# Performance work log

Measured on AMD Instinct MI355X. Metric: run time of the kernel, lower is better.

Reference implementation:

```python
import jax, jax.numpy as jnp
import numpy as np

B, T, A, H, E = 512, 64, 32, 512, 32


def sinusoidal_pos_encoding(t, dim):
    # t: (B, T) float positions -> (B, T, dim)
    half = dim // 2
    freqs = jnp.exp(-jnp.log(10000.0) * jnp.arange(half, dtype=jnp.float32) / half)
    ang = t[..., None] * freqs  # (B, T, half)
    return jnp.concatenate([jnp.sin(ang), jnp.cos(ang)], axis=-1)


def cat_linear(x, W, b, cat_ids):
    # x: (B, T, Din); W: (E, Din, Dout); b: (E, Dout); cat_ids: (B,)
    Wg = W[cat_ids]            # (B, Din, Dout) gathered per-sample weights
    bg = b[cat_ids][:, None]   # (B, 1, Dout)
    return jnp.einsum('btd,bdh->bth', x, Wg) + bg


def swish(x):
    return x * jax.nn.sigmoid(x)


def setup_inputs() -> dict:
    key = jax.random.key(0)
    ks = jax.random.split(key, 10)
    s = lambda fan_in: 1.0 / np.sqrt(fan_in)
    return {
        'actions': jax.random.normal(ks[0], (B, T, A), dtype=jnp.float32),
        'timesteps': jax.random.uniform(ks[1], (B,), dtype=jnp.float32),
        'cat_ids': jax.random.randint(ks[2], (B,), 0, E),
        'W1': jax.random.normal(ks[3], (E, A, H), dtype=jnp.float32) * s(A),
        'b1': jnp.zeros((E, H), dtype=jnp.float32),
        'W2': jax.random.normal(ks[4], (E, 2 * H, H), dtype=jnp.float32) * s(2 * H),
        'b2': jnp.zeros((E, H), dtype=jnp.float32),
        'W3': jax.random.normal(ks[5], (E, H, H), dtype=jnp.float32) * s(H),
        'b3': jnp.zeros((E, H), dtype=jnp.float32),
    }


def reference(actions, timesteps, cat_ids, W1, b1, W2, b2, W3, b3):
    b, t, _ = actions.shape
    timesteps_bt = jnp.broadcast_to(timesteps[:, None], (b, t))
    a_emb = cat_linear(actions, W1, b1, cat_ids)              # (B, T, H)
    tau_emb = sinusoidal_pos_encoding(timesteps_bt, H).astype(a_emb.dtype)
    x = jnp.concatenate([a_emb, tau_emb], axis=-1)            # (B, T, 2H)
    x = swish(cat_linear(x, W2, b2, cat_ids))                 # (B, T, H)
    x = cat_linear(x, W3, b3, cat_ids)                        # (B, T, H)
    return x
```

## Files before the change

kernel.cpp:

```cpp
#include <hip/hip_runtime.h>
#include <hip/hip_bf16.h>

#define B_ 512
#define T_ 64
#define A_ 32
#define H_ 512
#define E_ 32
#define MAX_TASKS 272
#define CAP_ 168
#define GRID_ (8 * CAP_)
#define SC 16

typedef unsigned short u16;
typedef unsigned int u32;
typedef __attribute__((ext_vector_type(8))) short short8;
typedef __attribute__((ext_vector_type(4))) float floatx4;

static __device__ __forceinline__ u16 f2bf(float f) {
    u32 u = __builtin_bit_cast(u32, f);
    u += 0x7fffu + ((u >> 16) & 1u);
    return (u16)(u >> 16);
}

static __device__ __forceinline__ void gl2lds16(const u16* g, u16* l) {
    __builtin_amdgcn_global_load_lds(
        (const __attribute__((address_space(1))) void*)g,
        (__attribute__((address_space(3))) void*)l, 16, 0, 0);
}

__global__ void group_kernel(const int* __restrict__ cat_ids,
                             int* __restrict__ sample_list,
                             int4* __restrict__ tasks,
                             int* __restrict__ itemlist,
                             int* __restrict__ eoff_g,
                             int* __restrict__ ecnt_g) {
    __shared__ int cnt[E_], off[E_], cur[E_], toff[E_], jc[8];
    __shared__ int total, fb;
    int tid = threadIdx.x;
    if (tid < E_) { cnt[tid] = 0; cur[tid] = 0; }
    __syncthreads();
    int e = cat_ids[tid];
    atomicAdd(&cnt[e], 1);
    __syncthreads();
    if (tid == 0) {
        int run = 0, trun = 0;
        for (int i = 0; i < E_; i++) {
            off[i] = run;  run += cnt[i];
            toff[i] = trun; trun += (cnt[i] + 1) >> 1;
        }
        total = trun;
    }
    __syncthreads();
    if (tid < E_) {
        int c = cnt[tid], o = off[tid], to = toff[tid];
        eoff_g[tid] = o;
        ecnt_g[tid] = c;
        for (int j = 0; j < c; j += 2)
            tasks[to++] = make_int4(tid, o + j, (c - j >= 2) ? 2 : 1, 0);
    }
    if (tid < 8) {
        int J = 0;
        for (int cc = 0; cc < 4; cc++) J += 4 * ((cnt[tid + 8 * cc] + 1) >> 1);
        jc[tid] = J;
    }
    __syncthreads();
    if (tid == 0) {
        int f = 0;
        for (int x = 0; x < 8; x++) if (jc[x] > CAP_) f = 1;
        fb = f;
    }
    __syncthreads();
    if (!fb) {
        if (tid < 8) {
            int j = 0;
            for (int cc = 0; cc < 4; cc++) {
                int ee = tid + 8 * cc;
                int nt = (cnt[ee] + 1) >> 1, t0 = toff[ee];
                for (int t = t0; t < t0 + nt; t++)
                    for (int nb = 0; nb < 4; nb++) {
                        itemlist[tid + 8 * j] = (t << 2) | nb;
                        j++;
                    }
            }
            for (; j < CAP_; j++) itemlist[tid + 8 * j] = -1;
        }
    } else {
        for (int f = tid; f < GRID_; f += 512)
            itemlist[f] = (f < 4 * total) ? f : -1;
    }
    int p = atomicAdd(&cur[e], 1);
    sample_list[off[e] + p] = tid;
}

__global__ __launch_bounds__(256) void embed_kernel(
        const float* __restrict__ actions, const int* __restrict__ cat_ids,
        const float* __restrict__ W1, const float* __restrict__ b1,
        u16* __restrict__ a_emb) {
    int b = blockIdx.x;
    int tid = threadIdx.x;
    int e = cat_ids[b];

    __shared__ float act[T_ * A_];
    const float* asrc = actions + (size_t)b * T_ * A_;
    for (int i = tid; i < T_ * A_; i += 256) act[i] = asrc[i];
    __syncthreads();

    const float* w1 = W1 + (size_t)e * A_ * H_;
    int n0 = tid, n1 = tid + 256;
    float wA[A_], wB[A_];
#pragma unroll
    for (int k = 0; k < A_; k++) {
        wA[k] = w1[k * H_ + n0];
        wB[k] = w1[k * H_ + n1];
    }
    float bA = b1[e * H_ + n0], bB = b1[e * H_ + n1];
    u16* orow = a_emb + (size_t)b * T_ * H_;
    for (int tt = 0; tt < T_; tt++) {
        float accA = bA, accB = bB;
#pragma unroll
        for (int k = 0; k < A_; k++) {
            float a = act[tt * A_ + k];
            accA = fmaf(a, wA[k], accA);
            accB = fmaf(a, wB[k], accB);
        }
        orow[tt * H_ + n0] = f2bf(accA);
        orow[tt * H_ + n1] = f2bf(accB);
    }
}

__global__ __launch_bounds__(256) void convert_transpose(
        const float* __restrict__ W, u16* __restrict__ Wt, int srcK, int dstK) {
    int n = blockIdx.y * 256 + threadIdx.x;
    int k0 = blockIdx.x * 32;
    int e = blockIdx.z;
    const float* src = W + ((size_t)e * srcK + k0) * H_ + n;
    short8 out[4];
#pragma unroll
    for (int j = 0; j < 32; j++)
        out[j >> 3][j & 7] = (short)f2bf(src[(size_t)j * H_]);
    u16* dst = Wt + ((size_t)e * H_ + n) * dstK + k0;
#pragma unroll
    for (int c = 0; c < 4; c++) *(short8*)(dst + c * 8) = out[c];
}

__global__ __launch_bounds__(256) void tau_bias_kernel(
        const float* __restrict__ W2, const float* __restrict__ b2,
        const float* __restrict__ timesteps, const int* __restrict__ sample_list,
        const int* __restrict__ eoff, const int* __restrict__ ecnt,
        float* __restrict__ bias2s) {
    int cc = blockIdx.x;
    int e = blockIdx.y;
    int cnt = ecnt[e], off = eoff[e];
    if (cnt == 0) return;
    int tid = threadIdx.x;
    int kq = tid >> 6, lane = tid & 63;
    int n = cc * 64 + lane;
    __shared__ float tauS[SC][512];
    __shared__ float pS[4][SC][64];
    const float* wb = W2 + ((size_t)e * 1024 + 512) * H_;

    for (int c0 = 0; c0 < cnt; c0 += SC) {
        for (int i = tid; i < SC * 512; i += 256) {
            int sl = i >> 9, k = i & 511;
            float v = 0.f;
            if (c0 + sl < cnt) {
                int s = sample_list[off + c0 + sl];
                float tval = timesteps[s];
                int kk = k & 255;
                float freq = expf(-9.210340371976184f * (float)kk * (1.0f / 256.0f));
                float ang = tval * freq;
                v = (k < 256) ? sinf(ang) : cosf(ang);
            }
            tauS[sl][k] = v;
        }
        __syncthreads();

        float a[SC];
#pragma unroll
        for (int s = 0; s < SC; s++) a[s] = 0.f;
        int kb = kq * 128;
        for (int k = kb; k < kb + 128; k += 4) {
            float w0 = wb[(size_t)k * H_ + n];
            float w1 = wb[(size_t)(k + 1) * H_ + n];
            float w2 = wb[(size_t)(k + 2) * H_ + n];
            float w3 = wb[(size_t)(k + 3) * H_ + n];
#pragma unroll
            for (int s = 0; s < SC; s++) {
                float4 t4 = *(const float4*)&tauS[s][k];
                a[s] = fmaf(t4.x, w0, a[s]);
                a[s] = fmaf(t4.y, w1, a[s]);
                a[s] = fmaf(t4.z, w2, a[s]);
                a[s] = fmaf(t4.w, w3, a[s]);
            }
        }
#pragma unroll
        for (int s = 0; s < SC; s++) pS[kq][s][lane] = a[s];
        __syncthreads();

        for (int o = tid; o < SC * 64; o += 256) {
            int sl = o >> 6, ln = o & 63;
            if (c0 + sl < cnt) {
                float v = pS[0][sl][ln] + pS[1][sl][ln] +
                          pS[2][sl][ln] + pS[3][sl][ln];
                int s = sample_list[off + c0 + sl];
                int col = cc * 64 + ln;
                bias2s[(size_t)s * H_ + col] = v + b2[e * H_ + col];
            }
        }
        __syncthreads();
    }
}

template <int DIN, bool PSBIAS, bool DO_SWISH, bool OUT_BF16>
__global__ __launch_bounds__(256, 2) void moe_gemm(
        const u16* __restrict__ xsrc, const u16* __restrict__ Wt,
        const float* __restrict__ bias,
        const int* __restrict__ sample_list, const int4* __restrict__ tasks,
        const int* __restrict__ itemlist, void* __restrict__ outp) {
    int item = itemlist[blockIdx.x];
    if (item < 0) return;
    int4 task = tasks[item >> 2];
    int nb = item & 3;
    int ns = task.z;
    int e = task.x;
    int s0 = sample_list[task.y];
    int s1 = (ns > 1) ? sample_list[task.y + 1] : s0;
    int n0 = nb * 128;

    int tid = threadIdx.x;
    int lane = tid & 63, wv = tid >> 6;
    int wr = wv >> 1, wc = wv & 1;
    int quad = lane >> 4, c15 = lane & 15;
    int r8 = lane >> 3, cg = lane & 7;

    __shared__ __align__(16) u16 xs[2][128 * 64];
    __shared__ __align__(16) u16 wt[2][128 * 64];

    floatx4 acc[4][4];
    floatx4 zero4 = {0.f, 0.f, 0.f, 0.f};
#pragma unroll
    for (int i = 0; i < 4; i++)
#pragma unroll
        for (int j = 0; j < 4; j++) acc[i][j] = zero4;

    const u16* wbase = Wt + (size_t)(e * H_ + n0) * DIN;
    int kc_sw = (cg ^ r8) * 8;

    auto stage = [&](int b, int k0) {
#pragma unroll
        for (int h = 0; h < 4; h++) {
            int rbase = h * 32 + wv * 8;
            int s = (h < 2) ? s0 : s1;
            int t = (rbase + r8) & 63;
            gl2lds16(xsrc + ((size_t)s * T_ + t) * H_ + k0 + kc_sw,
                     &xs[b][rbase * 64]);
        }
#pragma unroll
        for (int h = 0; h < 4; h++) {
            int nbase = h * 32 + wv * 8;
            gl2lds16(wbase + (size_t)(nbase + r8) * DIN + k0 + kc_sw,
                     &wt[b][nbase * 64]);
        }
    };

    auto compute = [&](int b) {
#pragma unroll
        for (int kk = 0; kk < 2; kk++) {
            int c = kk * 4 + quad;
            short8 af[4], bfr[4];
#pragma unroll
            for (int i = 0; i < 4; i++) {
                int row = wr * 64 + i * 16 + c15;
                af[i] = *(const short8*)&xs[b][row * 64 + ((c ^ (row & 7)) * 8)];
                int nr = wc * 64 + i * 16 + c15;
                bfr[i] = *(const short8*)&wt[b][nr * 64 + ((c ^ (nr & 7)) * 8)];
            }
#pragma unroll
            for (int mt = 0; mt < 4; mt++)
#pragma unroll
                for (int nt = 0; nt < 4; nt++)
                    acc[mt][nt] = __builtin_amdgcn_mfma_f32_16x16x32_bf16(
                            af[mt], bfr[nt], acc[mt][nt], 0, 0, 0);
        }
    };

    constexpr int KI = DIN / 64;
    stage(0, 0);
    __syncthreads();
#pragma unroll
    for (int t = 0; t < KI; ++t) {
        if (t + 1 < KI) stage((t + 1) & 1, (t + 1) * 64);
        compute(t & 1);
        if (t + 1 < KI) __syncthreads();
    }

    if (wr >= ns) return;
    int s = (wr == 0) ? s0 : s1;
    const float* bp = PSBIAS ? (bias + (size_t)s * H_)
                             : (bias + (size_t)e * H_);
#pragma unroll
    for (int mt = 0; mt < 4; mt++) {
        int tb = mt * 16 + quad * 4;
#pragma unroll
        for (int nt = 0; nt < 4; nt++) {
            int col = n0 + wc * 64 + nt * 16 + c15;
            float bv = bp[col];
#pragma unroll
            for (int r = 0; r < 4; r++) {
                float v = acc[mt][nt][r] + bv;
                if (DO_SWISH) v = v / (1.0f + expf(-v));
                size_t oidx = ((size_t)s * T_ + tb + r) * H_ + col;
                if (OUT_BF16) ((u16*)outp)[oidx] = f2bf(v);
                else          ((float*)outp)[oidx] = v;
            }
        }
    }
}

extern "C" void kernel_launch(void* const* d_in, const int* in_sizes, int n_in,
                              void* d_out, int out_size, void* d_ws, size_t ws_size,
                              hipStream_t stream) {
    const float* actions   = (const float*)d_in[0];
    const float* timesteps = (const float*)d_in[1];
    const int*   cat_ids   = (const int*)d_in[2];
    const float* W1 = (const float*)d_in[3];
    const float* b1 = (const float*)d_in[4];
    const float* W2 = (const float*)d_in[5];
    const float* b2 = (const float*)d_in[6];
    const float* W3 = (const float*)d_in[7];
    const float* b3 = (const float*)d_in[8];

    char* ws = (char*)d_ws;
    u16* a_emb = (u16*)ws;
    u16* y     = (u16*)(ws + (size_t)32 * 1024 * 1024);
    char* meta = ws + (size_t)64 * 1024 * 1024 + 512 * 1024;
    int*  sample_list = (int*)meta;
    int4* tasks       = (int4*)(meta + 8192);
    int*  itemlist    = (int*)(meta + 16384);
    int*  eoff        = (int*)(meta + 24576);
    int*  ecnt        = (int*)(meta + 24576 + 128);
    u16*  Wt2a   = (u16*)d_out;
    float* bias2s = (float*)((char*)d_out + (size_t)48 * 1024 * 1024);
    u16*  Wt3    = a_emb;

    hipLaunchKernelGGL(group_kernel, dim3(1), dim3(512), 0, stream,
                       cat_ids, sample_list, tasks, itemlist, eoff, ecnt);
    hipLaunchKernelGGL(embed_kernel, dim3(512), dim3(256), 0, stream,
                       actions, cat_ids, W1, b1, a_emb);
    hipLaunchKernelGGL(convert_transpose, dim3(H_ / 32, 2, E_), dim3(256),
                       0, stream, W2, Wt2a, 2 * H_, H_);
    hipLaunchKernelGGL(tau_bias_kernel, dim3(8, E_), dim3(256), 0, stream,
                       W2, b2, timesteps, sample_list, eoff, ecnt, bias2s);
    hipLaunchKernelGGL((moe_gemm<H_, true, true, true>), dim3(GRID_),
                       dim3(256), 0, stream,
                       a_emb, Wt2a, bias2s, sample_list, tasks, itemlist,
                       (void*)y);
    hipLaunchKernelGGL(convert_transpose, dim3(H_ / 32, 2, E_), dim3(256),
                       0, stream, W3, Wt3, H_, H_);
    hipLaunchKernelGGL((moe_gemm<H_, false, false, false>), dim3(GRID_),
                       dim3(256), 0, stream,
                       y, Wt3, b3, sample_list, tasks, itemlist, d_out);
}
```

Measured before the change: 328.2 us.

## Precompute tau embeddings once and restructure tau-bias matvec with transposed LDS

Sinusoidal tau features are now computed once per sample in the embed kernel and written to a scratch buffer in the output region. Previously they were recomputed in every tau-bias block, costing redundant transcendental math. The tau-bias kernel reads these from global memory into a transposed shared tile. Each thread now computes two output columns with interleaved k-strides, reducing across half-waves with shuffles. This amortizes W2 loads over more FMAs and lets tau values be read as float4s per k row, at the cost of an extra global buffer and more registers.

```diff
diff --git a/kernel.cpp b/kernel.cpp
--- a/kernel.cpp
+++ b/kernel.cpp
@@ -9,7 +9,7 @@
 #define MAX_TASKS 272
 #define CAP_ 168
 #define GRID_ (8 * CAP_)
-#define SC 16
+#define TSC 16
 
 typedef unsigned short u16;
 typedef unsigned int u32;
@@ -93,12 +93,21 @@
 }
 
 __global__ __launch_bounds__(256) void embed_kernel(
-        const float* __restrict__ actions, const int* __restrict__ cat_ids,
-        const float* __restrict__ W1, const float* __restrict__ b1,
-        u16* __restrict__ a_emb) {
+        const float* __restrict__ actions, const float* __restrict__ timesteps,
+        const int* __restrict__ cat_ids, const float* __restrict__ W1,
+        const float* __restrict__ b1, u16* __restrict__ a_emb,
+        float* __restrict__ tauG) {
     int b = blockIdx.x;
     int tid = threadIdx.x;
     int e = cat_ids[b];
+
+    {
+        float tval = timesteps[b];
+        float freq = expf(-9.210340371976184f * (float)tid * (1.0f / 256.0f));
+        float ang = tval * freq;
+        tauG[(size_t)b * H_ + tid]       = sinf(ang);
+        tauG[(size_t)b * H_ + 256 + tid] = cosf(ang);
+    }
 
     __shared__ float act[T_ * A_];
     const float* asrc = actions + (size_t)b * T_ * A_;
@@ -145,7 +154,7 @@
 
 __global__ __launch_bounds__(256) void tau_bias_kernel(
         const float* __restrict__ W2, const float* __restrict__ b2,
-        const float* __restrict__ timesteps, const int* __restrict__ sample_list,
+        const float* __restrict__ tauG, const int* __restrict__ sample_list,
         const int* __restrict__ eoff, const int* __restrict__ ecnt,
         float* __restrict__ bias2s) {
     int cc = blockIdx.x;
@@ -153,57 +162,66 @@
     int cnt = ecnt[e], off = eoff[e];
     if (cnt == 0) return;
     int tid = threadIdx.x;
-    int kq = tid >> 6, lane = tid & 63;
-    int n = cc * 64 + lane;
-    __shared__ float tauS[SC][512];
-    __shared__ float pS[4][SC][64];
+    int k8 = tid >> 5, ln = tid & 31;
+    int wv = tid >> 6;
+    int n0 = cc * 64 + ln, n1 = n0 + 32;
     const float* wb = W2 + ((size_t)e * 1024 + 512) * H_;
 
-    for (int c0 = 0; c0 < cnt; c0 += SC) {
-        for (int i = tid; i < SC * 512; i += 256) {
+    __shared__ float tauT[512][20];
+    __shared__ float pS[4][TSC][64];
+
+    for (int c0 = 0; c0 < cnt; c0 += TSC) {
+        for (int i = tid; i < TSC * 512; i += 256) {
             int sl = i >> 9, k = i & 511;
             float v = 0.f;
+            if (c0 + sl < cnt)
+                v = tauG[(size_t)sample_list[off + c0 + sl] * H_ + k];
+            tauT[k][sl] = v;
+        }
+        __syncthreads();
+
+        float a0[TSC], a1[TSC];
+#pragma unroll
+        for (int s = 0; s < TSC; s++) { a0[s] = 0.f; a1[s] = 0.f; }
+
+#pragma unroll 8
+        for (int j = 0; j < 64; j++) {
+            int k = k8 + j * 8;
+            float w0 = wb[(size_t)k * H_ + n0];
+            float w1 = wb[(size_t)k * H_ + n1];
+            float tv[TSC];
+            *(float4*)&tv[0]  = *(const float4*)&tauT[k][0];
+            *(float4*)&tv[4]  = *(const float4*)&tauT[k][4];
+            *(float4*)&tv[8]  = *(const float4*)&tauT[k][8];
+            *(float4*)&tv[12] = *(const float4*)&tauT[k][12];
+#pragma unroll
+            for (int s = 0; s < TSC; s++) {
+                a0[s] = fmaf(tv[s], w0, a0[s]);
+                a1[s] = fmaf(tv[s], w1, a1[s]);
+            }
+        }
+
+#pragma unroll
+        for (int s = 0; s < TSC; s++) {
+            a0[s] += __shfl_xor(a0[s], 32, 64);
+            a1[s] += __shfl_xor(a1[s], 32, 64);
+        }
+        if (!(tid & 32)) {
+#pragma unroll
+            for (int s = 0; s < TSC; s++) {
+                pS[wv][s][ln]      = a0[s];
+                pS[wv][s][ln + 32] = a1[s];
+            }
+        }
+        __syncthreads();
+
+        for (int o = tid; o < TSC * 64; o += 256) {
+            int sl = o >> 6, l = o & 63;
             if (c0 + sl < cnt) {
+                float v = pS[0][sl][l] + pS[1][sl][l] +
+                          pS[2][sl][l] + pS[3][sl][l];
                 int s = sample_list[off + c0 + sl];
-                float tval = timesteps[s];
-                int kk = k & 255;
-                float freq = expf(-9.210340371976184f * (float)kk * (1.0f / 256.0f));
-                float ang = tval * freq;
-                v = (k < 256) ? sinf(ang) : cosf(ang);
-            }
-            tauS[sl][k] = v;
-        }
-        __syncthreads();
-
-        float a[SC];
-#pragma unroll
-        for (int s = 0; s < SC; s++) a[s] = 0.f;
-        int kb = kq * 128;
-        for (int k = kb; k < kb + 128; k += 4) {
-            float w0 = wb[(size_t)k * H_ + n];
-            float w1 = wb[(size_t)(k + 1) * H_ + n];
-            float w2 = wb[(size_t)(k + 2) * H_ + n];
-            float w3 = wb[(size_t)(k + 3) * H_ + n];
-#pragma unroll
-            for (int s = 0; s < SC; s++) {
-                float4 t4 = *(const float4*)&tauS[s][k];
-                a[s] = fmaf(t4.x, w0, a[s]);
-                a[s] = fmaf(t4.y, w1, a[s]);
-                a[s] = fmaf(t4.z, w2, a[s]);
-                a[s] = fmaf(t4.w, w3, a[s]);
-            }
-        }
-#pragma unroll
-        for (int s = 0; s < SC; s++) pS[kq][s][lane] = a[s];
-        __syncthreads();
-
-        for (int o = tid; o < SC * 64; o += 256) {
-            int sl = o >> 6, ln = o & 63;
-            if (c0 + sl < cnt) {
-                float v = pS[0][sl][ln] + pS[1][sl][ln] +
-                          pS[2][sl][ln] + pS[3][sl][ln];
-                int s = sample_list[off + c0 + sl];
-                int col = cc * 64 + ln;
+                int col = cc * 64 + l;
                 bias2s[(size_t)s * H_ + col] = v + b2[e * H_ + col];
             }
         }
@@ -341,16 +359,17 @@
     int*  ecnt        = (int*)(meta + 24576 + 128);
     u16*  Wt2a   = (u16*)d_out;
     float* bias2s = (float*)((char*)d_out + (size_t)48 * 1024 * 1024);
+    float* tauG   = (float*)((char*)d_out + (size_t)52 * 1024 * 1024);
     u16*  Wt3    = a_emb;
 
     hipLaunchKernelGGL(group_kernel, dim3(1), dim3(512), 0, stream,
                        cat_ids, sample_list, tasks, itemlist, eoff, ecnt);
     hipLaunchKernelGGL(embed_kernel, dim3(512), dim3(256), 0, stream,
-                       actions, cat_ids, W1, b1, a_emb);
+                       actions, timesteps, cat_ids, W1, b1, a_emb, tauG);
     hipLaunchKernelGGL(convert_transpose, dim3(H_ / 32, 2, E_), dim3(256),
                        0, stream, W2, Wt2a, 2 * H_, H_);
     hipLaunchKernelGGL(tau_bias_kernel, dim3(8, E_), dim3(256), 0, stream,
-                       W2, b2, timesteps, sample_list, eoff, ecnt, bias2s);
+                       W2, b2, tauG, sample_list, eoff, ecnt, bias2s);
     hipLaunchKernelGGL((moe_gemm<H_, true, true, true>), dim3(GRID_),
                        dim3(256), 0, stream,
                        a_emb, Wt2a, bias2s, sample_list, tasks, itemlist,
```

Result: faster. 318.6 us (-2.9%).
